# Kernel optimization log

Measured on AMD Instinct MI355X. Metric: run time of the kernel, lower is better.

The kernel has to match this reference:

```python
import jax, jax.numpy as jnp
import numpy as np

B, L, DIN = 32, 512, 768
H, DH = 16, 48
DOUT = H * DH
NEG = 1e12


def setup_inputs() -> dict:
    key = jax.random.key(0)
    ks = jax.random.split(key, 8)
    lim = float(np.sqrt(6.0 / (DIN + DOUT)))  # xavier_uniform
    return {
        "Q_seq": jax.random.normal(ks[0], (B, L, DIN), jnp.float32),
        "K_seq": jax.random.normal(ks[1], (B, L, DIN), jnp.float32),
        "V_seq": jax.random.normal(ks[2], (B, L, DIN), jnp.float32),
        "WQ": jax.random.uniform(ks[3], (DIN, DOUT), jnp.float32, -lim, lim),
        "WK": jax.random.uniform(ks[4], (DIN, DOUT), jnp.float32, -lim, lim),
        "WV": jax.random.uniform(ks[5], (DIN, DOUT), jnp.float32, -lim, lim),
        "Q_len": jax.random.randint(ks[6], (B, 1), 0, L, jnp.int64),
        "V_len": jax.random.randint(ks[7], (B, 1), 0, L, jnp.int64),
    }


def reference(Q_seq, K_seq, V_seq, WQ, WK, WV, Q_len, V_len):
    b, l = Q_seq.shape[0], Q_seq.shape[1]
    # projections -> [B, H, L, DH]
    q = (Q_seq @ WQ).reshape(b, l, H, DH).transpose(0, 2, 1, 3)
    k = (K_seq @ WK).reshape(b, l, H, DH).transpose(0, 2, 1, 3)
    v = (V_seq @ WV).reshape(b, l, H, DH).transpose(0, 2, 1, 3)
    # scaled scores [B, H, Lq, Lk]
    A = jnp.einsum("bhqd,bhkd->bhqk", q, k) / jnp.sqrt(jnp.float32(DH))
    # key-length additive mask (original: scatter+cumsum == arange < len)
    mask_k = (jnp.arange(l) < V_len[:, 0][:, None]).astype(A.dtype)  # [B, Lk]
    A = A - (1.0 - mask_k)[:, None, None, :] * NEG
    # causal mask (mask_right=True): subtract on strictly upper triangle
    A = A - jnp.triu(jnp.ones((l, l), A.dtype), 1) * NEG
    A = jax.nn.softmax(A, axis=-1)
    # original quirk: O = A^T @ V  -> O[b,h,k,d] = sum_q A[b,h,q,k] V[b,h,q,d]
    O = jnp.einsum("bhqk,bhqd->bkhd", A, v).reshape(b, l, DOUT)
    # query-length multiplicative mask on output
    mask_q = (jnp.arange(l) < Q_len[:, 0][:, None]).astype(O.dtype)  # [B, L]
    return O * mask_q[:, :, None]
```

## Files before the change

kernel.cpp:

```cpp
#include <hip/hip_runtime.h>
#include <stdint.h>

#define B_    32
#define L_    512
#define DIN_  768
#define H_    16
#define DH_   48
#define DOUT_ 768
#define NHEADS (B_ * H_)
#define HEADELEMS (L_ * DH_)
#define MROWS (B_ * L_)

typedef short bf16x8 __attribute__((ext_vector_type(8)));
typedef float f32x4  __attribute__((ext_vector_type(4)));

__device__ __forceinline__ uint16_t f2bf(float f) {
  uint32_t u = __float_as_uint(f);
  u += 0x7fffu + ((u >> 16) & 1u);
  return (uint16_t)(u >> 16);
}
__device__ __forceinline__ uint32_t pack2bf(float lo, float hi) {
  uint32_t a = __float_as_uint(lo);
  a += 0x7fffu + ((a >> 16) & 1u);
  uint32_t b = __float_as_uint(hi);
  b += 0x7fffu + ((b >> 16) & 1u);
  return (a >> 16) | (b & 0xffff0000u);
}
__device__ __forceinline__ void gload_lds16(const void* g, void* l) {
  __builtin_amdgcn_global_load_lds(
      (const __attribute__((address_space(1))) uint32_t*)g,
      (__attribute__((address_space(3))) uint32_t*)l, 16, 0, 0);
}
__device__ __forceinline__ bf16x8 lds_frag8(const uint16_t* p) {
  union { uint2 u[2]; bf16x8 v; } x;
  x.u[0] = *(const uint2*)(p);
  x.u[1] = *(const uint2*)(p + 4);
  return x.v;
}

__global__ void lens_kernel(const int* __restrict__ qlen_raw,
                            const int* __restrict__ vlen_raw,
                            int* __restrict__ lens) {
  __shared__ int is64[2];
  int t = threadIdx.x;
  if (t < 2) {
    const int* src = (t == 0) ? qlen_raw : vlen_raw;
    int o = 0;
    for (int i = 0; i < 16; ++i) o |= src[2 * i + 1];
    is64[t] = (o == 0) ? 1 : 0;
  }
  __syncthreads();
  int which = t >> 5;
  int i = t & 31;
  const int* src = which ? vlen_raw : qlen_raw;
  lens[t] = is64[which] ? src[2 * i] : src[i];
}

__global__ void wconv_kernel(const float* __restrict__ WQ,
                             const float* __restrict__ WK,
                             const float* __restrict__ WV,
                             uint16_t* __restrict__ Wt) {
  const int z = blockIdx.z;
  const float* W = (z == 0) ? WQ : (z == 1) ? WK : WV;
  const float sc = (z == 0) ? 0.14433756729740643f : 1.0f;
  uint16_t* dst = Wt + (size_t)z * DIN_ * DOUT_;
  const int n  = blockIdx.x * 256 + threadIdx.x;
  const int k4 = blockIdx.y * 4;
  float f0 = W[(size_t)(k4 + 0) * DOUT_ + n] * sc;
  float f1 = W[(size_t)(k4 + 1) * DOUT_ + n] * sc;
  float f2 = W[(size_t)(k4 + 2) * DOUT_ + n] * sc;
  float f3 = W[(size_t)(k4 + 3) * DOUT_ + n] * sc;
  uint2 p;
  p.x = pack2bf(f0, f1);
  p.y = pack2bf(f2, f3);
  *(uint2*)&dst[(size_t)n * DIN_ + k4] = p;
}

__global__ void xconv_kernel(const float* __restrict__ Xq,
                             const float* __restrict__ Xk,
                             const float* __restrict__ Xv,
                             uint16_t* __restrict__ Xbf) {
  const int z = blockIdx.y;
  const float* src = (z == 0) ? Xq : (z == 1) ? Xk : Xv;
  uint16_t* dst = Xbf + (size_t)z * MROWS * DIN_;
  const size_t i = ((size_t)blockIdx.x * 256 + threadIdx.x) * 8;
  float4 x0 = *(const float4*)(src + i);
  float4 x1 = *(const float4*)(src + i + 4);
  uint4 p;
  p.x = pack2bf(x0.x, x0.y); p.y = pack2bf(x0.z, x0.w);
  p.z = pack2bf(x1.x, x1.y); p.w = pack2bf(x1.z, x1.w);
  *(uint4*)(dst + i) = p;
}

__global__ __launch_bounds__(512, 4) void mfma_proj(
    const uint16_t* __restrict__ Xbf, const uint16_t* __restrict__ Wt,
    uint16_t* __restrict__ qh, uint16_t* __restrict__ kh,
    uint16_t* __restrict__ vh) {
  const int z = blockIdx.z;
  const uint16_t* X = Xbf + (size_t)z * MROWS * DIN_;
  uint16_t* dst  = (z == 0) ? qh : (z == 1) ? kh : vh;
  const uint16_t* W = Wt + (size_t)z * DIN_ * DOUT_;

  __shared__ uint16_t As[128][32];
  __shared__ uint16_t Bs[256][32];

  const int t  = threadIdx.x;
  const int m0 = blockIdx.x * 128;
  const int n0 = blockIdx.y * 256;

  const int csw = ((t & 3) ^ ((t >> 3) & 3)) * 8;
  const uint16_t* aptr  = X + (size_t)(m0 + (t >> 2)) * DIN_ + csw;
  const uint16_t* bptr0 = W + (size_t)(n0 + (t >> 2)) * DIN_ + csw;
  const uint16_t* bptr1 = W + (size_t)(n0 + 128 + (t >> 2)) * DIN_ + csw;
  void* ldsA  = (char*)(&As[0][0]) + t * 16;
  void* ldsB0 = (char*)(&Bs[0][0]) + t * 16;
  void* ldsB1 = (char*)(&Bs[0][0]) + (t + 512) * 16;

  const int w = t >> 6, lane = t & 63;
  const int wm = (w & 1) * 64, wn = (w >> 1) * 64;
  const int fr = lane & 15;
  const int quad = lane >> 4;

  f32x4 acc[4][4];
#pragma unroll
  for (int i = 0; i < 4; ++i)
#pragma unroll
    for (int j = 0; j < 4; ++j) acc[i][j] = f32x4{0.f, 0.f, 0.f, 0.f};

  for (int kt = 0; kt < DIN_ / 32; ++kt) {
    const int k0 = kt * 32;
    gload_lds16(aptr + k0, ldsA);
    gload_lds16(bptr0 + k0, ldsB0);
    gload_lds16(bptr1 + k0, ldsB1);
    __syncthreads();

    bf16x8 af[4], bfr[4];
#pragma unroll
    for (int i = 0; i < 4; ++i) {
      const int r = wm + i * 16 + fr;
      af[i]  = *(const bf16x8*)&As[r][(quad ^ ((r >> 1) & 3)) * 8];
    }
#pragma unroll
    for (int j = 0; j < 4; ++j) {
      const int r = wn + j * 16 + fr;
      bfr[j] = *(const bf16x8*)&Bs[r][(quad ^ ((r >> 1) & 3)) * 8];
    }
#pragma unroll
    for (int mt = 0; mt < 4; ++mt)
#pragma unroll
      for (int nt = 0; nt < 4; ++nt)
        acc[mt][nt] = __builtin_amdgcn_mfma_f32_16x16x32_bf16(
            af[mt], bfr[nt], acc[mt][nt], 0, 0, 0);
    __syncthreads();
  }

#pragma unroll
  for (int mt = 0; mt < 4; ++mt) {
#pragma unroll
    for (int r = 0; r < 4; ++r) {
      const int m  = m0 + wm + mt * 16 + quad * 4 + r;
      const int bb = m >> 9;
      const int l  = m & 511;
#pragma unroll
      for (int nt = 0; nt < 4; ++nt) {
        const int n = n0 + wn + nt * 16 + fr;
        const int h = n / DH_;
        const int d = n - h * DH_;
        dst[(((size_t)bb * H_ + h) * L_ + l) * DH_ + d] = f2bf(acc[mt][nt][r]);
      }
    }
  }
}

__global__ __launch_bounds__(256, 2) void attn_mfma(
    const uint16_t* __restrict__ qh, const uint16_t* __restrict__ kh,
    const uint16_t* __restrict__ vh, const int* __restrict__ lens,
    float* __restrict__ out) {
  const int bh = blockIdx.x;
  const int b  = bh >> 4;
  const int h  = bh & 15;
  const int t    = threadIdx.x;
  const int w    = t >> 6;
  const int lane = t & 63;
  const int l15  = lane & 15;
  const int quad = lane >> 4;

  const int qlen = lens[b];
  const int vlen = lens[32 + b];
  const bool deg = (vlen == 0);
  const size_t head = (size_t)bh * HEADELEMS;

  __shared__ uint16_t Pt[4][128][36];
  __shared__ uint16_t Vt[48][36];
  __shared__ float    prt[4][32];

  const uint16_t* qbase = qh + head;
  const uint16_t* kbase = kh + head;
  const uint16_t* vbase = vh + head;

  f32x4 Oacc[8][3];
#pragma unroll
  for (int i = 0; i < 8; ++i)
#pragma unroll
    for (int dt = 0; dt < 3; ++dt) Oacc[i][dt] = f32x4{0.f, 0.f, 0.f, 0.f};

  for (int g = 0; g < 16; ++g) {
    const int q0 = g * 32;
    const int lim = q0 + 31 - 16 * w;

    __syncthreads();

    if (t < 192) {
      const int vq = t & 31, oct = t >> 5;
      uint4 u = *(const uint4*)(vbase + (size_t)(q0 + vq) * DH_ + oct * 8);
      const int d0 = oct * 8;
      Vt[d0 + 0][vq] = (uint16_t)(u.x);
      Vt[d0 + 1][vq] = (uint16_t)(u.x >> 16);
      Vt[d0 + 2][vq] = (uint16_t)(u.y);
      Vt[d0 + 3][vq] = (uint16_t)(u.y >> 16);
      Vt[d0 + 4][vq] = (uint16_t)(u.z);
      Vt[d0 + 5][vq] = (uint16_t)(u.z >> 16);
      Vt[d0 + 6][vq] = (uint16_t)(u.w);
      Vt[d0 + 7][vq] = (uint16_t)(u.w >> 16);
    }

    bf16x8 aq[2][2];
#pragma unroll
    for (int mt = 0; mt < 2; ++mt) {
      const uint16_t* qp = qbase + (size_t)(q0 + mt * 16 + l15) * DH_;
      aq[mt][0] = *(const bf16x8*)(qp + quad * 8);
      bf16x8 zz = {0, 0, 0, 0, 0, 0, 0, 0};
      aq[mt][1] = zz;
      if (quad < 2) aq[mt][1] = *(const bf16x8*)(qp + 32 + quad * 8);
    }

    float lrun[2][4];
#pragma unroll
    for (int mt = 0; mt < 2; ++mt)
#pragma unroll
      for (int r = 0; r < 4; ++r) lrun[mt][r] = 0.0f;

#pragma unroll
    for (int i = 0; i < 8; ++i) {
      if (64 * i > lim) continue;
      const int kb = 64 * i + 16 * w;
      f32x4 s0 = {0.f, 0.f, 0.f, 0.f};
      f32x4 s1 = {0.f, 0.f, 0.f, 0.f};
      if (!deg) {
        const uint16_t* kp = kbase + (size_t)(kb + l15) * DH_;
        bf16x8 bk0 = *(const bf16x8*)(kp + quad * 8);
        bf16x8 bk1 = {0, 0, 0, 0, 0, 0, 0, 0};
        if (quad < 2) bk1 = *(const bf16x8*)(kp + 32 + quad * 8);
        s0 = __builtin_amdgcn_mfma_f32_16x16x32_bf16(aq[0][0], bk0, s0, 0, 0, 0);
        s0 = __builtin_amdgcn_mfma_f32_16x16x32_bf16(aq[0][1], bk1, s0, 0, 0, 0);
        s1 = __builtin_amdgcn_mfma_f32_16x16x32_bf16(aq[1][0], bk0, s1, 0, 0, 0);
        s1 = __builtin_amdgcn_mfma_f32_16x16x32_bf16(aq[1][1], bk1, s1, 0, 0, 0);
      }
      const int kc  = kb + l15;
      const int row = i * 16 + l15;
#pragma unroll
      for (int mt = 0; mt < 2; ++mt) {
        f32x4 sv = (mt == 0) ? s0 : s1;
        float p4[4];
#pragma unroll
        for (int r = 0; r < 4; ++r) {
          const int qrow = q0 + mt * 16 + quad * 4 + r;
          float e;
          if (deg) {
            e = (kc <= qrow) ? 1.0f : 0.0f;
          } else {
            e = (kc < vlen && kc <= qrow) ? __expf(sv[r]) : 0.0f;
          }
          lrun[mt][r] += e;
          p4[r] = e;
        }
        const int col = mt * 16 + quad * 4;
        *(uint32_t*)&Pt[w][row][col]     = pack2bf(p4[0], p4[1]);
        *(uint32_t*)&Pt[w][row][col + 2] = pack2bf(p4[2], p4[3]);
      }
    }

#pragma unroll
    for (int mt = 0; mt < 2; ++mt)
#pragma unroll
      for (int r = 0; r < 4; ++r) {
        float l = lrun[mt][r];
#pragma unroll
        for (int off = 1; off < 16; off <<= 1) l += __shfl_xor(l, off, 64);
        lrun[mt][r] = l;
      }
    if (l15 == 0) {
#pragma unroll
      for (int mt = 0; mt < 2; ++mt)
#pragma unroll
        for (int r = 0; r < 4; ++r)
          prt[w][mt * 16 + quad * 4 + r] = lrun[mt][r];
    }
    __syncthreads();

    {
      const int q = t & 31;
      const float inv = __builtin_amdgcn_rcpf(
          prt[0][q] + prt[1][q] + prt[2][q] + prt[3][q]);
#pragma unroll
      for (int j = 0; j < 6; ++j) {
        const int d = (t >> 5) + 8 * j;
        float f = __uint_as_float((uint32_t)Vt[d][q] << 16) * inv;
        Vt[d][q] = f2bf(f);
      }
    }
    __syncthreads();

    bf16x8 bv[3];
#pragma unroll
    for (int dt = 0; dt < 3; ++dt)
      bv[dt] = lds_frag8(&Vt[dt * 16 + l15][quad * 8]);
#pragma unroll
    for (int i = 0; i < 8; ++i) {
      if (64 * i > lim) continue;
      bf16x8 ap = lds_frag8(&Pt[w][i * 16 + l15][quad * 8]);
#pragma unroll
      for (int dt = 0; dt < 3; ++dt)
        Oacc[i][dt] = __builtin_amdgcn_mfma_f32_16x16x32_bf16(
            ap, bv[dt], Oacc[i][dt], 0, 0, 0);
    }
  }

#pragma unroll
  for (int i = 0; i < 8; ++i) {
#pragma unroll
    for (int r = 0; r < 4; ++r) {
      const int k_abs = 64 * i + 16 * w + quad * 4 + r;
      const float msk = (k_abs < qlen) ? 1.0f : 0.0f;
      float* orow = out + (size_t)(b * L_ + k_abs) * DOUT_ + h * DH_;
#pragma unroll
      for (int dt = 0; dt < 3; ++dt)
        orow[dt * 16 + l15] = Oacc[i][dt][r] * msk;
    }
  }
}

extern "C" void kernel_launch(void* const* d_in, const int* in_sizes, int n_in,
                              void* d_out, int out_size, void* d_ws, size_t ws_size,
                              hipStream_t stream) {
  const float* Qs  = (const float*)d_in[0];
  const float* Kse = (const float*)d_in[1];
  const float* Vs  = (const float*)d_in[2];
  const float* WQ  = (const float*)d_in[3];
  const float* WK  = (const float*)d_in[4];
  const float* WV  = (const float*)d_in[5];
  const int*   Qlen = (const int*)d_in[6];
  const int*   Vlen = (const int*)d_in[7];
  float* out = (float*)d_out;

  char* ws = (char*)d_ws;
  int* lens = (int*)ws;
  uint16_t* qh  = (uint16_t*)(ws + 256);
  uint16_t* kh  = qh + (size_t)B_ * H_ * L_ * DH_;
  uint16_t* vh  = kh + (size_t)B_ * H_ * L_ * DH_;
  uint16_t* Wt  = vh + (size_t)B_ * H_ * L_ * DH_;
  uint16_t* Xbf = Wt + (size_t)3 * DIN_ * DOUT_;

  lens_kernel<<<1, 64, 0, stream>>>(Qlen, Vlen, lens);
  wconv_kernel<<<dim3(3, 192, 3), 256, 0, stream>>>(WQ, WK, WV, Wt);
  xconv_kernel<<<dim3(MROWS * DIN_ / 2048, 3), 256, 0, stream>>>(Qs, Kse, Vs, Xbf);
  mfma_proj<<<dim3(MROWS / 128, DOUT_ / 256, 3), 512, 0, stream>>>(
      Xbf, Wt, qh, kh, vh);
  attn_mfma<<<NHEADS, 256, 0, stream>>>(qh, kh, vh, lens, out);
}
```

Measured before the change: 343.5 us.

## Fuse fp32-to-bf16 input conversion into projection GEMM with double-buffered LDS

Removes the separate xconv kernel and has the projection GEMM load fp32 activations straight into LDS, converting them to bf16 in registers with v_cvt_pk_bf16_f32 before the MFMA. This drops a full write and re-read of the bf16 activation copy. It also adds double-buffered LDS staging, so the next k-tile's loads are issued while the current tile is computed. In exchange the A tile doubles in LDS footprint and global read bytes, and the conversion is repeated by every N-block (three per row block).

Measured after the change: 339.8 us. No clear change (-1.1%).

```diff
diff --git a/kernel.cpp b/kernel.cpp
--- a/kernel.cpp
+++ b/kernel.cpp
@@ -76,50 +76,51 @@
   *(uint2*)&dst[(size_t)n * DIN_ + k4] = p;
 }
 
-__global__ void xconv_kernel(const float* __restrict__ Xq,
-                             const float* __restrict__ Xk,
-                             const float* __restrict__ Xv,
-                             uint16_t* __restrict__ Xbf) {
-  const int z = blockIdx.y;
-  const float* src = (z == 0) ? Xq : (z == 1) ? Xk : Xv;
-  uint16_t* dst = Xbf + (size_t)z * MROWS * DIN_;
-  const size_t i = ((size_t)blockIdx.x * 256 + threadIdx.x) * 8;
-  float4 x0 = *(const float4*)(src + i);
-  float4 x1 = *(const float4*)(src + i + 4);
-  uint4 p;
-  p.x = pack2bf(x0.x, x0.y); p.y = pack2bf(x0.z, x0.w);
-  p.z = pack2bf(x1.x, x1.y); p.w = pack2bf(x1.z, x1.w);
-  *(uint4*)(dst + i) = p;
-}
-
 __global__ __launch_bounds__(512, 4) void mfma_proj(
-    const uint16_t* __restrict__ Xbf, const uint16_t* __restrict__ Wt,
+    const float* __restrict__ Xq, const float* __restrict__ Xk,
+    const float* __restrict__ Xv, const uint16_t* __restrict__ Wt,
     uint16_t* __restrict__ qh, uint16_t* __restrict__ kh,
     uint16_t* __restrict__ vh) {
   const int z = blockIdx.z;
-  const uint16_t* X = Xbf + (size_t)z * MROWS * DIN_;
+  const float* X = (z == 0) ? Xq : (z == 1) ? Xk : Xv;
   uint16_t* dst  = (z == 0) ? qh : (z == 1) ? kh : vh;
   const uint16_t* W = Wt + (size_t)z * DIN_ * DOUT_;
 
-  __shared__ uint16_t As[128][32];
-  __shared__ uint16_t Bs[256][32];
+  __shared__ float    Asf[2][128][32];
+  __shared__ uint16_t Bs[2][256][32];
 
   const int t  = threadIdx.x;
   const int m0 = blockIdx.x * 128;
   const int n0 = blockIdx.y * 256;
 
-  const int csw = ((t & 3) ^ ((t >> 3) & 3)) * 8;
-  const uint16_t* aptr  = X + (size_t)(m0 + (t >> 2)) * DIN_ + csw;
-  const uint16_t* bptr0 = W + (size_t)(n0 + (t >> 2)) * DIN_ + csw;
-  const uint16_t* bptr1 = W + (size_t)(n0 + 128 + (t >> 2)) * DIN_ + csw;
-  void* ldsA  = (char*)(&As[0][0]) + t * 16;
-  void* ldsB0 = (char*)(&Bs[0][0]) + t * 16;
-  void* ldsB1 = (char*)(&Bs[0][0]) + (t + 512) * 16;
+  const int arow = t >> 3;
+  const int achk = (t & 7) ^ (arow & 7);
+  const float* aptr0 = X + (size_t)(m0 + arow) * DIN_ + achk * 4;
+  const float* aptr1 = aptr0 + (size_t)64 * DIN_;
+
+  const int bcsw = ((t & 3) ^ ((t >> 3) & 3)) * 8;
+  const uint16_t* bptr0 = W + (size_t)(n0 + (t >> 2)) * DIN_ + bcsw;
+  const uint16_t* bptr1 = W + (size_t)(n0 + 128 + (t >> 2)) * DIN_ + bcsw;
+
+  char* aB = (char*)&Asf[0][0][0] + t * 16;
+  char* bB = (char*)&Bs[0][0][0] + t * 16;
+
+#define STAGE_(buf_, kt_)                                   \
+  {                                                         \
+    const int k0_ = (kt_) * 32;                             \
+    gload_lds16(aptr0 + k0_, aB + (buf_) * 16384);          \
+    gload_lds16(aptr1 + k0_, aB + (buf_) * 16384 + 8192);   \
+    gload_lds16(bptr0 + k0_, bB + (buf_) * 16384);          \
+    gload_lds16(bptr1 + k0_, bB + (buf_) * 16384 + 8192);   \
+  }
 
   const int w = t >> 6, lane = t & 63;
   const int wm = (w & 1) * 64, wn = (w >> 1) * 64;
   const int fr = lane & 15;
   const int quad = lane >> 4;
+  const int rx  = fr & 7;
+  const int ac0 = ((2 * quad)     ^ rx) * 4;
+  const int ac1 = ((2 * quad + 1) ^ rx) * 4;
 
   f32x4 acc[4][4];
 #pragma unroll
@@ -127,32 +128,37 @@
 #pragma unroll
     for (int j = 0; j < 4; ++j) acc[i][j] = f32x4{0.f, 0.f, 0.f, 0.f};
 
+  STAGE_(0, 0);
+  __syncthreads();
+  int cur = 0;
   for (int kt = 0; kt < DIN_ / 32; ++kt) {
-    const int k0 = kt * 32;
-    gload_lds16(aptr + k0, ldsA);
-    gload_lds16(bptr0 + k0, ldsB0);
-    gload_lds16(bptr1 + k0, ldsB1);
-    __syncthreads();
-
-    bf16x8 af[4], bfr[4];
-#pragma unroll
-    for (int i = 0; i < 4; ++i) {
-      const int r = wm + i * 16 + fr;
-      af[i]  = *(const bf16x8*)&As[r][(quad ^ ((r >> 1) & 3)) * 8];
-    }
+    if (kt + 1 < DIN_ / 32) STAGE_(cur ^ 1, kt + 1);
+
+    bf16x8 bfr[4];
 #pragma unroll
     for (int j = 0; j < 4; ++j) {
       const int r = wn + j * 16 + fr;
-      bfr[j] = *(const bf16x8*)&Bs[r][(quad ^ ((r >> 1) & 3)) * 8];
-    }
-#pragma unroll
-    for (int mt = 0; mt < 4; ++mt)
+      bfr[j] = *(const bf16x8*)&Bs[cur][r][(quad ^ ((r >> 1) & 3)) * 8];
+    }
+#pragma unroll
+    for (int mt = 0; mt < 4; ++mt) {
+      const float* ar = &Asf[cur][wm + mt * 16 + fr][0];
+      float4 a0 = *(const float4*)(ar + ac0);
+      float4 a1 = *(const float4*)(ar + ac1);
+      union { uint32_t u[4]; bf16x8 v; } cv;
+      asm("v_cvt_pk_bf16_f32 %0, %1, %2" : "=v"(cv.u[0]) : "v"(a0.x), "v"(a0.y));
+      asm("v_cvt_pk_bf16_f32 %0, %1, %2" : "=v"(cv.u[1]) : "v"(a0.z), "v"(a0.w));
+      asm("v_cvt_pk_bf16_f32 %0, %1, %2" : "=v"(cv.u[2]) : "v"(a1.x), "v"(a1.y));
+      asm("v_cvt_pk_bf16_f32 %0, %1, %2" : "=v"(cv.u[3]) : "v"(a1.z), "v"(a1.w));
 #pragma unroll
       for (int nt = 0; nt < 4; ++nt)
         acc[mt][nt] = __builtin_amdgcn_mfma_f32_16x16x32_bf16(
-            af[mt], bfr[nt], acc[mt][nt], 0, 0, 0);
+            cv.v, bfr[nt], acc[mt][nt], 0, 0, 0);
+    }
     __syncthreads();
-  }
+    cur ^= 1;
+  }
+#undef STAGE_
 
 #pragma unroll
   for (int mt = 0; mt < 4; ++mt) {
@@ -359,12 +365,10 @@
   uint16_t* kh  = qh + (size_t)B_ * H_ * L_ * DH_;
   uint16_t* vh  = kh + (size_t)B_ * H_ * L_ * DH_;
   uint16_t* Wt  = vh + (size_t)B_ * H_ * L_ * DH_;
-  uint16_t* Xbf = Wt + (size_t)3 * DIN_ * DOUT_;
 
   lens_kernel<<<1, 64, 0, stream>>>(Qlen, Vlen, lens);
   wconv_kernel<<<dim3(3, 192, 3), 256, 0, stream>>>(WQ, WK, WV, Wt);
-  xconv_kernel<<<dim3(MROWS * DIN_ / 2048, 3), 256, 0, stream>>>(Qs, Kse, Vs, Xbf);
   mfma_proj<<<dim3(MROWS / 128, DOUT_ / 256, 3), 512, 0, stream>>>(
-      Xbf, Wt, qh, kh, vh);
+      Qs, Kse, Vs, Wt, qh, kh, vh);
   attn_mfma<<<NHEADS, 256, 0, stream>>>(qh, kh, vh, lens, out);
 }
```
